# Kernel optimization log

Hardware: AMD Instinct MI355X
Metric: run time of the kernel (lower is better)

Reference implementation:

```python
import jax, jax.numpy as jnp
import numpy as np

B, T, E, H, VF, C = 4, 8192, 512, 8, 2, 256
KD = E // H          # key dim per head = 64
HD = E * VF // H     # value head dim = 128


def _rel_pos():
    decay = np.log(1.0 - 2.0 ** (-5.0 - np.arange(H, dtype=np.float64)))  # [H]
    ang = 1.0 / (10000 ** np.linspace(0, 1, KD // 2))
    ang = np.repeat(ang, 2)                                  # [KD]
    idx = np.arange(T)
    sin = np.sin(idx[:, None] * ang[None, :]).astype(np.float32)
    cos = np.cos(idx[:, None] * ang[None, :]).astype(np.float32)
    bi = np.arange(C)
    diff = bi[:, None] - bi[None, :]
    m = np.where(diff >= 0, np.exp(decay[:, None, None] * diff), 0.0)  # [H,C,C]
    last = m[:, -1]                                          # [H,C]
    vid = (last / last.sum(-1, keepdims=True))[:, :, None]   # [H,C,1]
    scale = np.sqrt(m.sum(-1, keepdims=True))                # [H,C,1]
    mask = (m / scale).astype(np.float32)
    cross_decay = np.exp(decay * C)[:, None, None].astype(np.float32)  # [H,1,1]
    qid = np.exp(decay[:, None] * (bi + 1))[:, :, None]      # [H,C,1]
    qid = (qid / (scale / last.sum(-1)[:, None, None])).astype(np.float32)
    return sin, cos, mask, cross_decay, qid, vid.astype(np.float32)


def setup_inputs() -> dict:
    key = jax.random.key(0)
    ks = jax.random.split(key, 6)
    sin, cos, mask, cross_decay, qid, vid = _rel_pos()
    s = 0.02
    return {
        'x': jax.random.normal(ks[0], (B, T, E), jnp.float32),
        'sin': jnp.asarray(sin), 'cos': jnp.asarray(cos),
        'mask': jnp.asarray(mask), 'cross_decay': jnp.asarray(cross_decay),
        'query_inner_decay': jnp.asarray(qid), 'value_inner_decay': jnp.asarray(vid),
        'Wq': jax.random.normal(ks[1], (E, E), jnp.float32) * s,
        'Wk': jax.random.normal(ks[2], (E, E), jnp.float32) * s,
        'Wv': jax.random.normal(ks[3], (E, E * VF), jnp.float32) * s,
        'Wg': jax.random.normal(ks[4], (E, E * VF), jnp.float32) * s,
        'Wo': jax.random.normal(ks[5], (E * VF, E), jnp.float32) * s,
    }


def _rotate_every_two(x):
    x1, x2 = x[..., ::2], x[..., 1::2]
    return jnp.stack((-x2, x1), axis=-1).reshape(x.shape)


def _theta_shift(x, sin, cos):
    return x * cos + _rotate_every_two(x) * sin


def reference(x, sin, cos, mask, cross_decay, query_inner_decay, value_inner_decay, Wq, Wk, Wv, Wg, Wo):
    Bz, Tl, _ = x.shape
    q = (x @ Wq).reshape(Bz, Tl, H, KD).transpose(0, 2, 1, 3)               # [B,H,T,KD]
    k = ((x @ Wk) * (KD ** -0.5)).reshape(Bz, Tl, H, KD).transpose(0, 2, 1, 3)
    v = x @ Wv                                                              # [B,T,E*VF]
    g = x @ Wg
    qr = _theta_shift(q, sin, cos)
    kr = _theta_shift(k, sin, cos)

    NC = Tl // C
    qr = qr.reshape(Bz, H, NC, C, KD).transpose(0, 2, 1, 3, 4)              # [B,NC,H,C,KD]
    kr = kr.reshape(Bz, H, NC, C, KD).transpose(0, 2, 1, 3, 4)
    vc = v.reshape(Bz, NC, C, H, HD).transpose(0, 1, 3, 2, 4)               # [B,NC,H,C,HD]

    qk = jnp.einsum('bnhck,bnhdk->bnhcd', qr, kr) * mask                    # decay-masked intra-chunk
    inner_scale = jnp.clip(jax.lax.stop_gradient(jnp.abs(qk)).sum(-1, keepdims=True), 1.0, None)
    qk = qk / inner_scale
    inner_output = jnp.einsum('bnhcd,bnhde->bnhce', qk, vc)                 # [B,NC,H,C,HD]

    kv = jnp.einsum('bnhck,bnhcd->bnhkd', kr, vc * value_inner_decay)       # [B,NC,H,KD,HD]

    def step(carry, kv_i):
        kv_state, kv_scale = carry
        out = (kv_state / kv_scale, kv_scale)
        kv_state = kv_state * cross_decay + kv_i
        kv_scale = jnp.clip(
            jax.lax.stop_gradient(jnp.abs(kv_state)).sum(-2, keepdims=True).max(-1, keepdims=True),
            1.0, None)
        return (kv_state, kv_scale), out

    kv_state0 = jnp.zeros((Bz, H, KD, HD), x.dtype)
    kv_scale0 = jnp.ones((Bz, H, 1, 1), x.dtype)
    _, (kv_recurrent, cross_scale) = jax.lax.scan(step, (kv_state0, kv_scale0), jnp.swapaxes(kv, 0, 1))
    kv_recurrent = jnp.swapaxes(kv_recurrent, 0, 1)                         # [B,NC,H,KD,HD]
    cross_scale = jnp.swapaxes(cross_scale, 0, 1)                           # [B,NC,H,1,1]

    all_scale = jnp.maximum(inner_scale, cross_scale)
    cross_output = jnp.einsum('bnhck,bnhkd->bnhcd', qr * query_inner_decay, kv_recurrent)
    output = inner_output / (all_scale / inner_scale) + cross_output / (all_scale / cross_scale)
    output = output.transpose(0, 1, 3, 2, 4)                                # [B,NC,C,H,HD]
    # group_norm: RMSNorm over head_dim, no affine
    output = output * jax.lax.rsqrt(jnp.mean(output ** 2, -1, keepdims=True) + 1e-6)
    output = output.reshape(Bz, Tl, H * HD)
    output = jax.nn.silu(g) * output
    return output @ Wo
```

## Files before the change

kernel.cpp:

```cpp
#include <hip/hip_runtime.h>
#include <cmath>

#define Bz 4
#define Tt 8192
#define Ee 512
#define Hh 8
#define Cc 256
#define KD 64
#define HD 128
#define NC 32
#define EV 1024
#define Mrows (Bz*Tt)

typedef unsigned short u16;
typedef __attribute__((ext_vector_type(4))) float f32x4;
typedef __attribute__((ext_vector_type(8))) short s16x8;

__device__ __forceinline__ u16 f2b(float f) {
    union { float f; unsigned u; } v; v.f = f;
    unsigned r = v.u + 0x7FFFu + ((v.u >> 16) & 1u);
    return (u16)(r >> 16);
}
__device__ __forceinline__ float b2f(u16 u) {
    union { unsigned u; float f; } v; v.u = ((unsigned)u) << 16;
    return v.f;
}
#define MFMA16(a, b, c) __builtin_amdgcn_mfma_f32_16x16x32_bf16((a), (b), (c), 0, 0, 0)

__device__ __forceinline__ size_t fpk(int row, int k, int K) {
    return (size_t)(row >> 4) * (K * 16) + (k >> 5) * 512 + ((k >> 3) & 3) * 128 +
           (row & 15) * 8 + (k & 7);
}

__global__ __launch_bounds__(256) void cast_x_k(const float* __restrict__ x,
                                                u16* __restrict__ xb) {
    size_t i = ((size_t)blockIdx.x * 256 + threadIdx.x) * 4;
    float4 v = *(const float4*)(x + i);
    int m = (int)(i >> 9), e = (int)(i & 511);
    ushort4 o;
    o.x = f2b(v.x); o.y = f2b(v.y); o.z = f2b(v.z); o.w = f2b(v.w);
    *(ushort4*)(xb + fpk(m, e, 512)) = o;
}

__global__ __launch_bounds__(256) void castT_k(const float* __restrict__ W,
                                               u16* __restrict__ Wt,
                                               int K, int N, float scale) {
    __shared__ float tile[32][33];
    int k0 = blockIdx.y * 32, n0 = blockIdx.x * 32;
    int r = threadIdx.x >> 3, c4 = (threadIdx.x & 7) * 4;
    float4 v = *(const float4*)(W + (size_t)(k0 + r) * N + n0 + c4);
    tile[r][c4] = v.x; tile[r][c4 + 1] = v.y; tile[r][c4 + 2] = v.z; tile[r][c4 + 3] = v.w;
    __syncthreads();
    ushort4 o;
    o.x = f2b(tile[c4 + 0][r] * scale);
    o.y = f2b(tile[c4 + 1][r] * scale);
    o.z = f2b(tile[c4 + 2][r] * scale);
    o.w = f2b(tile[c4 + 3][r] * scale);
    *(ushort4*)(Wt + fpk(n0 + r, k0 + c4, K)) = o;
}

template <int EPI>
__global__ __launch_bounds__(256) void gemm_mfma(const u16* __restrict__ A,
                                                 const u16* __restrict__ Bt,
                                                 void* __restrict__ Cout,
                                                 int K, int N,
                                                 const float* __restrict__ sn,
                                                 const float* __restrict__ cs) {
    int tid = threadIdx.x;
    int lane = tid & 63, wid = tid >> 6;
    int cL = lane & 15, quad = lane >> 4;
    int m0 = blockIdx.y * 128 + (wid & 1) * 64;
    int n0 = blockIdx.x * 128 + (wid >> 1) * 64;
    const int KT = K * 16;
    f32x4 acc[4][4] = {};
    for (int k0 = 0; k0 < K; k0 += 32) {
        s16x8 af[4], bfr[4];
        size_t ko = (size_t)(k0 >> 5) * 512 + quad * 128 + cL * 8;
        #pragma unroll
        for (int mt = 0; mt < 4; ++mt)
            af[mt] = *(const s16x8*)(A + (size_t)((m0 >> 4) + mt) * KT + ko);
        #pragma unroll
        for (int nt = 0; nt < 4; ++nt)
            bfr[nt] = *(const s16x8*)(Bt + (size_t)((n0 >> 4) + nt) * KT + ko);
        #pragma unroll
        for (int mt = 0; mt < 4; ++mt)
            #pragma unroll
            for (int nt = 0; nt < 4; ++nt)
                acc[mt][nt] = MFMA16(af[mt], bfr[nt], acc[mt][nt]);
    }
    if (EPI == 0) {
        u16* dst = (u16*)Cout;
        #pragma unroll
        for (int mt = 0; mt < 4; ++mt)
            #pragma unroll
            for (int nt = 0; nt < 4; ++nt)
                #pragma unroll
                for (int i = 0; i < 4; ++i) {
                    int m = m0 + mt * 16 + quad * 4 + i;
                    int n = n0 + nt * 16 + cL;
                    float v = acc[mt][nt][i];
                    float p = __shfl_xor(v, 1, 64);
                    int t = m & 8191, b = m >> 13, h = n >> 6, kd = n & 63;
                    float c1 = cs[t * 64 + kd], s1 = sn[t * 64 + kd];
                    float o = (n & 1) ? (v * c1 + p * s1) : (v * c1 - p * s1);
                    dst[(size_t)(b * 8 + h) * 524288 + fpk(t, kd, 64)] = f2b(o);
                }
    } else if (EPI == 1) {
        u16* vt = (u16*)Cout;
        #pragma unroll
        for (int mt = 0; mt < 4; ++mt)
            #pragma unroll
            for (int nt = 0; nt < 4; ++nt) {
                int m = m0 + mt * 16 + quad * 4;
                int n = n0 + nt * 16 + cL;
                int b = m >> 13, t = m & 8191;
                int nn = t >> 8, ccc = t & 255;
                int h = n >> 7, e = n & 127;
                ushort4 pk;
                pk.x = f2b(acc[mt][nt][0]);
                pk.y = f2b(acc[mt][nt][1]);
                pk.z = f2b(acc[mt][nt][2]);
                pk.w = f2b(acc[mt][nt][3]);
                *(ushort4*)(vt + (((size_t)((b * 8 + h) * 32 + nn)) << 15) +
                            fpk(e, ccc, 256)) = pk;
            }
    } else if (EPI == 2) {
        u16* dst = (u16*)Cout;
        #pragma unroll
        for (int mt = 0; mt < 4; ++mt)
            #pragma unroll
            for (int nt = 0; nt < 4; ++nt)
                #pragma unroll
                for (int i = 0; i < 4; ++i) {
                    int m = m0 + mt * 16 + quad * 4 + i;
                    int n = n0 + nt * 16 + cL;
                    dst[fpk(m, n, N)] = f2b(acc[mt][nt][i]);
                }
    } else {
        float* dst = (float*)Cout;
        #pragma unroll
        for (int mt = 0; mt < 4; ++mt)
            #pragma unroll
            for (int nt = 0; nt < 4; ++nt)
                #pragma unroll
                for (int i = 0; i < 4; ++i)
                    dst[(size_t)(m0 + mt * 16 + quad * 4 + i) * N + n0 + nt * 16 + cL] =
                        acc[mt][nt][i];
    }
}

__global__ __launch_bounds__(256) void attn_mfma(const u16* __restrict__ qr,
                                                 const u16* __restrict__ kr,
                                                 const u16* __restrict__ vt,
                                                 const float* __restrict__ mask,
                                                 u16* __restrict__ ATT,
                                                 float* __restrict__ iscale_g) {
    __shared__ u16 Ss[64][264];
    __shared__ float partial[4][64];
    __shared__ float sInvL[64];
    int p = blockIdx.x;
    int g = (p & 7) | ((p >> 5) << 3);
    int rtile = (p >> 3) & 3;
    int h = g & 7; int n = (g >> 3) & 31; int b = g >> 8;
    int tid = threadIdx.x, lane = tid & 63, w = tid >> 6;
    int cL = lane & 15, quad = lane >> 4;

    size_t qf_bh = (size_t)(b * 8 + h) * 524288;
    f32x4 acc[4][4] = {};
    if (w <= rtile) {
        const u16* Qb = qr + qf_bh + (size_t)(n * 16 + rtile * 4) * 1024;
        const u16* Kb = kr + qf_bh + (size_t)(n * 16 + w * 4) * 1024;
        #pragma unroll
        for (int kt = 0; kt < 2; ++kt) {
            s16x8 af[4], bfr[4];
            size_t ko = (size_t)kt * 512 + quad * 128 + cL * 8;
            #pragma unroll
            for (int mt = 0; mt < 4; ++mt)
                af[mt] = *(const s16x8*)(Qb + (size_t)mt * 1024 + ko);
            #pragma unroll
            for (int nt = 0; nt < 4; ++nt)
                bfr[nt] = *(const s16x8*)(Kb + (size_t)nt * 1024 + ko);
            #pragma unroll
            for (int mt = 0; mt < 4; ++mt)
                #pragma unroll
                for (int nt = 0; nt < 4; ++nt)
                    acc[mt][nt] = MFMA16(af[mt], bfr[nt], acc[mt][nt]);
        }
    }
    float rs[4][4] = {};
    if (w <= rtile) {
        const float* mb = mask + ((size_t)h << 16);
        #pragma unroll
        for (int mt = 0; mt < 4; ++mt)
            #pragma unroll
            for (int nt = 0; nt < 4; ++nt)
                #pragma unroll
                for (int i = 0; i < 4; ++i) {
                    int r = rtile * 64 + mt * 16 + quad * 4 + i;
                    int d = w * 64 + nt * 16 + cL;
                    float s = acc[mt][nt][i] * mb[r * 256 + d];
                    Ss[mt * 16 + quad * 4 + i][w * 64 + nt * 16 + cL] = f2b(s);
                    rs[mt][i] += fabsf(s);
                }
    }
    #pragma unroll
    for (int mt = 0; mt < 4; ++mt)
        #pragma unroll
        for (int i = 0; i < 4; ++i) {
            float v = rs[mt][i];
            v += __shfl_xor(v, 1, 16);
            v += __shfl_xor(v, 2, 16);
            v += __shfl_xor(v, 4, 16);
            v += __shfl_xor(v, 8, 16);
            if (cL == 0) partial[w][mt * 16 + quad * 4 + i] = v;
        }
    __syncthreads();
    if (tid < 64) {
        float tot = partial[0][tid] + partial[1][tid] + partial[2][tid] + partial[3][tid];
        tot = fmaxf(tot, 1.f);
        iscale_g[((size_t)((b * 32 + n) * 8 + h)) * 256 + rtile * 64 + tid] = tot;
        sInvL[tid] = 1.f / tot;
    }
    __syncthreads();

    f32x4 o[8] = {};
    const u16* Vb = vt + (((size_t)((b * 8 + h) * 32 + n)) << 15);
    int kmax = 2 * (rtile + 1);
    for (int kt = 0; kt < kmax; ++kt) {
        s16x8 a = *(const s16x8*)(&Ss[w * 16 + cL][kt * 32 + quad * 8]);
        #pragma unroll
        for (int nt = 0; nt < 8; ++nt) {
            s16x8 bv = *(const s16x8*)(Vb + (size_t)nt * 4096 + kt * 512 +
                                       quad * 128 + cL * 8);
            o[nt] = MFMA16(a, bv, o[nt]);
        }
    }
    size_t obase = ((size_t)b * 8192 + n * 256 + rtile * 64) * 1024 + h * 128;
    #pragma unroll
    for (int nt = 0; nt < 8; ++nt)
        #pragma unroll
        for (int i = 0; i < 4; ++i) {
            int row = w * 16 + quad * 4 + i;
            ATT[obase + (size_t)row * 1024 + nt * 16 + cL] = f2b(o[nt][i] * sInvL[row]);
        }
}

__global__ __launch_bounds__(256) void chunkkv_mfma(const u16* __restrict__ kr,
                                                    const u16* __restrict__ vt,
                                                    const float* __restrict__ vid,
                                                    float* __restrict__ kvT) {
    __shared__ u16 KtL[64][264];
    int bid = blockIdx.x;
    int h = bid & 7; bid >>= 3;
    int n = bid & 31; int b = bid >> 5;
    int tid = threadIdx.x, lane = tid & 63, w = tid >> 6;
    int cL = lane & 15, quad = lane >> 4;
    size_t qf_bh = (size_t)(b * 8 + h) * 524288;
    {
        int c = tid;
        const u16* rp = kr + qf_bh + (size_t)(n * 16 + (c >> 4)) * 1024 + (c & 15) * 8;
        #pragma unroll
        for (int u = 0; u < 8; ++u) {
            s16x8 vv = *(const s16x8*)(rp + (u >> 2) * 512 + (u & 3) * 128);
            #pragma unroll
            for (int j = 0; j < 8; ++j) KtL[u * 8 + j][c] = (u16)vv[j];
        }
    }
    __syncthreads();
    const u16* Vb = vt + (((size_t)((b * 8 + h) * 32 + n)) << 15);
    f32x4 acc[2][4] = {};
    for (int kt = 0; kt < 8; ++kt) {
        float vidv[8];
        #pragma unroll
        for (int j = 0; j < 8; ++j) vidv[j] = vid[h * 256 + kt * 32 + quad * 8 + j];
        s16x8 af[2];
        #pragma unroll
        for (int mt = 0; mt < 2; ++mt) {
            s16x8 raw = *(const s16x8*)(Vb + (size_t)(w * 2 + mt) * 4096 +
                                        kt * 512 + quad * 128 + cL * 8);
            #pragma unroll
            for (int j = 0; j < 8; ++j)
                af[mt][j] = (short)f2b(b2f((u16)raw[j]) * vidv[j]);
        }
        #pragma unroll
        for (int nt = 0; nt < 4; ++nt) {
            s16x8 bv = *(const s16x8*)(&KtL[nt * 16 + cL][kt * 32 + quad * 8]);
            #pragma unroll
            for (int mt = 0; mt < 2; ++mt) acc[mt][nt] = MFMA16(af[mt], bv, acc[mt][nt]);
        }
    }
    float* out = kvT + ((size_t)((b * 32 + n) * 8 + h)) * 8192;
    #pragma unroll
    for (int mt = 0; mt < 2; ++mt)
        #pragma unroll
        for (int nt = 0; nt < 4; ++nt)
            #pragma unroll
            for (int i = 0; i < 4; ++i)
                out[(w * 32 + mt * 16 + quad * 4 + i) * 64 + nt * 16 + cL] = acc[mt][nt][i];
}

__global__ __launch_bounds__(256) void scan_par(const float* __restrict__ kvT,
                                                u16* __restrict__ kvrecb,
                                                const float* __restrict__ cdv,
                                                float* __restrict__ cscale) {
    int bid = blockIdx.x;
    int n = bid & 31; bid >>= 5;
    int h = bid & 7; int b = bid >> 3;
    int tid = threadIdx.x, lane = tid & 63, g = tid >> 6;
    float cd = cdv[h];
    float st[32];
    #pragma unroll
    for (int i = 0; i < 32; ++i) st[i] = 0.f;
    for (int j = 0; j < n; ++j) {
        size_t base = ((size_t)((b * 32 + j) * 8 + h)) * 8192;
        #pragma unroll
        for (int i = 0; i < 32; ++i) {
            int e = g + 4 * i;
            st[i] = st[i] * cd + kvT[base + e * 64 + lane];
        }
    }
    __shared__ float esum[128];
    __shared__ float sSc;
    #pragma unroll
    for (int i = 0; i < 32; ++i) {
        float s = fabsf(st[i]);
        s += __shfl_xor(s, 1, 64);
        s += __shfl_xor(s, 2, 64);
        s += __shfl_xor(s, 4, 64);
        s += __shfl_xor(s, 8, 64);
        s += __shfl_xor(s, 16, 64);
        s += __shfl_xor(s, 32, 64);
        if (lane == 0) esum[g + 4 * i] = s;
    }
    __syncthreads();
    if (tid < 64) {
        float m1 = fmaxf(esum[tid], esum[tid + 64]);
        m1 = fmaxf(m1, __shfl_xor(m1, 1, 64));
        m1 = fmaxf(m1, __shfl_xor(m1, 2, 64));
        m1 = fmaxf(m1, __shfl_xor(m1, 4, 64));
        m1 = fmaxf(m1, __shfl_xor(m1, 8, 64));
        m1 = fmaxf(m1, __shfl_xor(m1, 16, 64));
        m1 = fmaxf(m1, __shfl_xor(m1, 32, 64));
        if (tid == 0) sSc = fmaxf(m1, 1.f);
    }
    __syncthreads();
    float scale = sSc;
    float inv = 1.f / scale;
    size_t baseN = ((size_t)((b * 32 + n) * 8 + h)) * 8192;
    #pragma unroll
    for (int i = 0; i < 32; ++i) {
        int e = g + 4 * i;
        kvrecb[baseN + ((size_t)(lane >> 3) * 128 + e) * 8 + (lane & 7)] = f2b(st[i] * inv);
    }
    if (tid == 0) cscale[(b * 32 + n) * 8 + h] = scale;
}

__global__ __launch_bounds__(256) void cross_mfma(const u16* __restrict__ qr,
                                                  const u16* __restrict__ kvrecb,
                                                  const float* __restrict__ iscale_g,
                                                  const float* __restrict__ cscale_g,
                                                  const float* __restrict__ qid,
                                                  u16* __restrict__ ATT) {
    int bid = blockIdx.x;
    int h = bid & 7; bid >>= 3;
    int n = bid & 31; int b = bid >> 5;
    int tid = threadIdx.x, lane = tid & 63, w = tid >> 6;
    int cL = lane & 15, quad = lane >> 4;
    size_t qf_bh = (size_t)(b * 8 + h) * 524288;
    const u16* Qb = qr + qf_bh + (size_t)(n * 16 + w * 4) * 1024;
    const u16* KVb = kvrecb + ((size_t)((b * 32 + n) * 8 + h)) * 8192;
    s16x8 af[4][2];
    #pragma unroll
    for (int mt = 0; mt < 4; ++mt)
        #pragma unroll
        for (int kt = 0; kt < 2; ++kt)
            af[mt][kt] = *(const s16x8*)(Qb + (size_t)mt * 1024 + kt * 512 +
                                         quad * 128 + cL * 8);
    float csc = cscale_g[(b * 32 + n) * 8 + h];
    size_t ibase = ((size_t)((b * 32 + n) * 8 + h)) * 256 + w * 64;
    size_t obase = ((size_t)(b * 8192 + n * 256 + w * 64)) * 1024 + h * 128;
    #pragma unroll
    for (int hn = 0; hn < 2; ++hn) {
        f32x4 acc[4][4] = {};
        #pragma unroll
        for (int kt = 0; kt < 2; ++kt)
            #pragma unroll
            for (int nt = 0; nt < 4; ++nt) {
                int e = (hn * 4 + nt) * 16 + cL;
                s16x8 bv = *(const s16x8*)(KVb + ((size_t)(kt * 4 + quad) * 128 + e) * 8);
                #pragma unroll
                for (int mt = 0; mt < 4; ++mt)
                    acc[mt][nt] = MFMA16(af[mt][kt], bv, acc[mt][nt]);
            }
        #pragma unroll
        for (int mt = 0; mt < 4; ++mt)
            #pragma unroll
            for (int i = 0; i < 4; ++i) {
                int r = mt * 16 + quad * 4 + i;
                float isc = iscale_g[ibase + r];
                float alls = fmaxf(isc, csc);
                float qdv = qid[h * 256 + w * 64 + r];
                float fI = isc / alls;
                float fC = (csc / alls) * qdv;
                #pragma unroll
                for (int nt = 0; nt < 4; ++nt) {
                    int e = (hn * 4 + nt) * 16 + cL;
                    size_t oi = obase + (size_t)r * 1024 + e;
                    float prev = b2f(ATT[oi]);
                    ATT[oi] = f2b(prev * fI + acc[mt][nt][i] * fC);
                }
            }
    }
}

__global__ __launch_bounds__(256) void rms_silu(const u16* __restrict__ ATT,
                                                u16* __restrict__ g) {
    __shared__ u16 att_s[16 * 1036];
    __shared__ float rmsv[16][8];
    int tile = blockIdx.x;
    int tid = threadIdx.x;
    size_t abase = (size_t)tile * 16 * 1024;
    int head = tid >> 5;
    #pragma unroll
    for (int jj = 0; jj < 16; ++jj) {
        ushort4 v = *(const ushort4*)(ATT + abase + (size_t)jj * 1024 + tid * 4);
        *(ushort4*)(att_s + jj * 1036 + tid * 4) = v;
        float x0 = b2f(v.x), x1 = b2f(v.y), x2 = b2f(v.z), x3 = b2f(v.w);
        float ss = x0 * x0 + x1 * x1 + x2 * x2 + x3 * x3;
        ss += __shfl_xor(ss, 1, 32);
        ss += __shfl_xor(ss, 2, 32);
        ss += __shfl_xor(ss, 4, 32);
        ss += __shfl_xor(ss, 8, 32);
        ss += __shfl_xor(ss, 16, 32);
        if ((tid & 31) == 0)
            rmsv[jj][head] = rsqrtf(ss * (1.f / 128.f) + 1e-6f);
    }
    __syncthreads();
    size_t gbase = (size_t)tile * 16384;
    #pragma unroll
    for (int it = 0; it < 16; ++it) {
        int p = it * 1024 + tid * 4;
        int e = ((p >> 9) << 5) | (((p >> 7) & 3) << 3) | (p & 7);
        int r = (p >> 3) & 15;
        ushort4 gv = *(const ushort4*)(g + gbase + p);
        ushort4 av = *(const ushort4*)(att_s + r * 1036 + e);
        float rms = rmsv[r][e >> 7];
        float x0 = b2f(av.x), x1 = b2f(av.y), x2 = b2f(av.z), x3 = b2f(av.w);
        float g0 = b2f(gv.x), g1 = b2f(gv.y), g2 = b2f(gv.z), g3 = b2f(gv.w);
        ushort4 ov;
        ov.x = f2b((g0 / (1.f + __expf(-g0))) * x0 * rms);
        ov.y = f2b((g1 / (1.f + __expf(-g1))) * x1 * rms);
        ov.z = f2b((g2 / (1.f + __expf(-g2))) * x2 * rms);
        ov.w = f2b((g3 / (1.f + __expf(-g3))) * x3 * rms);
        *(ushort4*)(g + gbase + p) = ov;
    }
}

extern "C" void kernel_launch(void* const* d_in, const int* in_sizes, int n_in,
                              void* d_out, int out_size, void* d_ws, size_t ws_size,
                              hipStream_t stream) {
    const float* x    = (const float*)d_in[0];
    const float* sn   = (const float*)d_in[1];
    const float* cs   = (const float*)d_in[2];
    const float* mask = (const float*)d_in[3];
    const float* cdv  = (const float*)d_in[4];
    const float* qid  = (const float*)d_in[5];
    const float* vid  = (const float*)d_in[6];
    const float* Wq   = (const float*)d_in[7];
    const float* Wk   = (const float*)d_in[8];
    const float* Wv   = (const float*)d_in[9];
    const float* Wg   = (const float*)d_in[10];
    const float* Wo   = (const float*)d_in[11];
    float* out = (float*)d_out;

    char* w = (char*)d_ws;
    u16* qr     = (u16*)w;   w += (size_t)16777216 * 2;
    u16* kr     = (u16*)w;   w += (size_t)16777216 * 2;
    u16* vt     = (u16*)w;   w += (size_t)33554432 * 2;
    u16* xbf    = (u16*)w;   w += (size_t)16777216 * 2;
    u16* wqT    = (u16*)w;   w += (size_t)262144 * 2;
    u16* wkT    = (u16*)w;   w += (size_t)262144 * 2;
    u16* wvT    = (u16*)w;   w += (size_t)524288 * 2;
    u16* wgT    = (u16*)w;   w += (size_t)524288 * 2;
    u16* woT    = (u16*)w;   w += (size_t)524288 * 2;
    float* kvT  = (float*)w; w += (size_t)8388608 * 4;
    u16* kvrecb = (u16*)w;   w += (size_t)8388608 * 2;
    float* iscale = (float*)w; w += (size_t)262144 * 4;
    float* cscale = (float*)w; w += (size_t)1024 * 4;

    u16* gbuf = qr;
    u16* ATT  = (u16*)d_out;

    dim3 blk(256);
    cast_x_k<<<dim3(16384), blk, 0, stream>>>(x, xbf);
    castT_k<<<dim3(16, 16), blk, 0, stream>>>(Wq, wqT, 512, 512, 1.0f);
    castT_k<<<dim3(16, 16), blk, 0, stream>>>(Wk, wkT, 512, 512, 0.125f);
    castT_k<<<dim3(32, 16), blk, 0, stream>>>(Wv, wvT, 512, 1024, 1.0f);
    castT_k<<<dim3(32, 16), blk, 0, stream>>>(Wg, wgT, 512, 1024, 1.0f);
    castT_k<<<dim3(16, 32), blk, 0, stream>>>(Wo, woT, 1024, 512, 1.0f);
    gemm_mfma<0><<<dim3(4, 256), blk, 0, stream>>>(xbf, wqT, qr, 512, 512, sn, cs);
    gemm_mfma<0><<<dim3(4, 256), blk, 0, stream>>>(xbf, wkT, kr, 512, 512, sn, cs);
    gemm_mfma<1><<<dim3(8, 256), blk, 0, stream>>>(xbf, wvT, vt, 512, 1024, nullptr, nullptr);
    attn_mfma<<<dim3(4096), blk, 0, stream>>>(qr, kr, vt, mask, ATT, iscale);
    chunkkv_mfma<<<dim3(1024), blk, 0, stream>>>(kr, vt, vid, kvT);
    scan_par<<<dim3(1024), blk, 0, stream>>>(kvT, kvrecb, cdv, cscale);
    cross_mfma<<<dim3(1024), blk, 0, stream>>>(qr, kvrecb, iscale, cscale, qid, ATT);
    gemm_mfma<2><<<dim3(8, 256), blk, 0, stream>>>(xbf, wgT, gbuf, 512, 1024, nullptr, nullptr);
    rms_silu<<<dim3(2048), blk, 0, stream>>>(ATT, gbuf);
    gemm_mfma<3><<<dim3(4, 256), blk, 0, stream>>>(gbuf, woT, out, 1024, 512, nullptr, nullptr);
}
```

Before: 673.2 us.

## Stage GEMM operand tiles through double-buffered LDS via direct global-to-LDS loads

The MFMA GEMM previously had each wave load its A and B fragments straight from global memory, so tiles shared between waves were fetched redundantly. Each block now cooperatively copies the 128x32 A and B chunks into a double-buffered shared-memory tile using global_load_lds. The next K chunk is prefetched while the current one feeds the MFMAs. This adds 32 KB of LDS per block and a barrier every K step, which may reduce occupancy and adds sync overhead.

```diff
diff --git a/kernel.cpp b/kernel.cpp
--- a/kernel.cpp
+++ b/kernel.cpp
@@ -27,6 +27,13 @@
 }
 #define MFMA16(a, b, c) __builtin_amdgcn_mfma_f32_16x16x32_bf16((a), (b), (c), 0, 0, 0)
 
+__device__ __forceinline__ void glds16(const u16* g, u16* l) {
+    __builtin_amdgcn_global_load_lds(
+        (const __attribute__((address_space(1))) unsigned int*)g,
+        (__attribute__((address_space(3))) unsigned int*)l,
+        16, 0, 0);
+}
+
 __device__ __forceinline__ size_t fpk(int row, int k, int K) {
     return (size_t)(row >> 4) * (K * 16) + (k >> 5) * 512 + ((k >> 3) & 3) * 128 +
            (row & 15) * 8 + (k & 7);
@@ -66,28 +73,53 @@
                                                  int K, int N,
                                                  const float* __restrict__ sn,
                                                  const float* __restrict__ cs) {
+    __shared__ u16 lds[2][8192];
     int tid = threadIdx.x;
     int lane = tid & 63, wid = tid >> 6;
     int cL = lane & 15, quad = lane >> 4;
+    int M0 = blockIdx.y * 8, N0 = blockIdx.x * 8;
     int m0 = blockIdx.y * 128 + (wid & 1) * 64;
     int n0 = blockIdx.x * 128 + (wid >> 1) * 64;
     const int KT = K * 16;
+    const int NK = K >> 5;
+
+#define STAGE(buf, kc) do {                                                        \
+        size_t kofs = (size_t)(kc) * 512 + lane * 8;                               \
+        glds16(A  + (size_t)(M0 + wid * 2    ) * KT + kofs,                        \
+               &lds[buf][(wid * 2    ) * 512]);                                    \
+        glds16(A  + (size_t)(M0 + wid * 2 + 1) * KT + kofs,                        \
+               &lds[buf][(wid * 2 + 1) * 512]);                                    \
+        glds16(Bt + (size_t)(N0 + wid * 2    ) * KT + kofs,                        \
+               &lds[buf][4096 + (wid * 2    ) * 512]);                             \
+        glds16(Bt + (size_t)(N0 + wid * 2 + 1) * KT + kofs,                        \
+               &lds[buf][4096 + (wid * 2 + 1) * 512]);                             \
+    } while (0)
+
+    STAGE(0, 0);
+    __syncthreads();
+
     f32x4 acc[4][4] = {};
-    for (int k0 = 0; k0 < K; k0 += 32) {
+    int mh = (wid & 1) * 4, nh = (wid >> 1) * 4;
+    for (int kc = 0; kc < NK; ++kc) {
+        int cur = kc & 1;
+        if (kc + 1 < NK) STAGE(cur ^ 1, kc + 1);
         s16x8 af[4], bfr[4];
-        size_t ko = (size_t)(k0 >> 5) * 512 + quad * 128 + cL * 8;
-        #pragma unroll
-        for (int mt = 0; mt < 4; ++mt)
-            af[mt] = *(const s16x8*)(A + (size_t)((m0 >> 4) + mt) * KT + ko);
+        int fo = quad * 128 + cL * 8;
+        #pragma unroll
+        for (int mt = 0; mt < 4; ++mt)
+            af[mt] = *(const s16x8*)(&lds[cur][(mh + mt) * 512 + fo]);
         #pragma unroll
         for (int nt = 0; nt < 4; ++nt)
-            bfr[nt] = *(const s16x8*)(Bt + (size_t)((n0 >> 4) + nt) * KT + ko);
+            bfr[nt] = *(const s16x8*)(&lds[cur][4096 + (nh + nt) * 512 + fo]);
         #pragma unroll
         for (int mt = 0; mt < 4; ++mt)
             #pragma unroll
             for (int nt = 0; nt < 4; ++nt)
                 acc[mt][nt] = MFMA16(af[mt], bfr[nt], acc[mt][nt]);
-    }
+        __syncthreads();
+    }
+#undef STAGE
+
     if (EPI == 0) {
         u16* dst = (u16*)Cout;
         #pragma unroll
```

Result: faster. 654.6 us (-2.7%).
